# Kernel tuning notes

Hardware: AMD Instinct MI355X
Metric: run time of the kernel (lower is better)

The kernel has to match this reference:

```python
import jax, jax.numpy as jnp
import numpy as np

NUM_EXPERTS = 4


def setup_inputs() -> dict:
    key = jax.random.key(0)
    k1, k2, k3 = jax.random.split(key, 3)
    B, N, H = 8, 2048, 2048
    E = NUM_EXPERTS
    I = H * 4 // E  # expert_intermediate_size = 2048
    x = jax.random.normal(k1, (B, N, H), dtype=jnp.float32)
    gate_up_proj = jax.random.normal(k2, (E, H, 2 * I), dtype=jnp.float32) * 0.02
    down_proj = jax.random.normal(k3, (E, I, H), dtype=jnp.float32) * 0.02
    return {"x": x, "gate_up_proj": gate_up_proj, "down_proj": down_proj}


def reference(x, gate_up_proj, down_proj):
    # Token-routed MLP with deterministic routing: expert(pos) = pos % E.
    # Instead of gathering full weight matrices per token (as the torch code
    # does), group tokens by expert via a reshape: pos = g*E + e -> expert e.
    B, N, H = x.shape
    E, _, two_I = gate_up_proj.shape
    I = two_I // 2
    G = N // E
    x4 = x.reshape(B, G, E, H)
    # gate+up projection, grouped GEMM over expert axis e
    gu = jnp.einsum('bgeh,ehd->bged', x4, gate_up_proj)  # [B,G,E,2I]
    gate, up = gu[..., :I], gu[..., I:]
    inter = jax.nn.silu(gate) * up  # SwiGLU, [B,G,E,I]
    out = jnp.einsum('bgei,eih->bgeh', inter, down_proj)  # [B,G,E,H]
    return out.reshape(B, N, H)
```

## Files before the change

### kernel.cpp

```cpp
#include <hip/hip_runtime.h>

#define HDIM 2048
#define IDIM 2048
#define KD   2048
#define ME   4096
#define NT   64


typedef __bf16 bf16x8 __attribute__((ext_vector_type(8)));
typedef float f32x4 __attribute__((ext_vector_type(4)));

__device__ __forceinline__ unsigned short f2bf(float f) {
  unsigned u = __builtin_bit_cast(unsigned, f);
  u += 0x7FFFu + ((u >> 16) & 1u);
  return (unsigned short)(u >> 16);
}

__device__ __forceinline__ void gld16(const void* g, void* l) {
  __builtin_amdgcn_global_load_lds(
      (const __attribute__((address_space(1))) unsigned int*)g,
      (__attribute__((address_space(3))) unsigned int*)l, 16, 0, 0);
}

template<int N> __device__ __forceinline__ void wait_vmcnt() {
  asm volatile("s_waitcnt vmcnt(%0)" :: "i"(N) : "memory");
}

__global__ void __launch_bounds__(256) pack_x(const float* __restrict__ x,
                                              unsigned short* __restrict__ xb) {
  const int row = blockIdx.x;
  const int n = row & 2047;
  const int b = row >> 11;
  const int e = n & 3, g = n >> 2;
  const float4* src = (const float4*)(x + (size_t)row * HDIM);
  unsigned short* dst = xb + ((size_t)e * ME + b * 512 + g) * HDIM;
  const int t = threadIdx.x;
  float4 v0 = src[2 * t];
  float4 v1 = src[2 * t + 1];
  uint4 pk;
  pk.x = (unsigned)f2bf(v0.x) | ((unsigned)f2bf(v0.y) << 16);
  pk.y = (unsigned)f2bf(v0.z) | ((unsigned)f2bf(v0.w) << 16);
  pk.z = (unsigned)f2bf(v1.x) | ((unsigned)f2bf(v1.y) << 16);
  pk.w = (unsigned)f2bf(v1.z) | ((unsigned)f2bf(v1.w) << 16);
  *(uint4*)(dst + 8 * t) = pk;
}

__global__ void __launch_bounds__(256) transpose_cvt(const float* __restrict__ src,
                                                     unsigned short* __restrict__ dst,
                                                     int R, int C) {
  __shared__ unsigned short tile[32][33];
  const size_t eo = (size_t)blockIdx.z * R * C;
  src += eo;
  dst += eo;
  const int c0 = blockIdx.x * 32, r0 = blockIdx.y * 32;
  const int tx = threadIdx.x & 31, ty = threadIdx.x >> 5;
#pragma unroll
  for (int j = 0; j < 4; ++j) {
    int r = r0 + ty + j * 8;
    tile[ty + j * 8][tx] = f2bf(src[(size_t)r * C + c0 + tx]);
  }
  __syncthreads();
#pragma unroll
  for (int j = 0; j < 4; ++j) {
    int c = c0 + ty + j * 8;
    dst[(size_t)c * R + r0 + tx] = tile[tx][ty + j * 8];
  }
}


template<int VMN, bool STG>
__device__ __forceinline__ void g1_tile(const unsigned short* S, int ab0, int bb0,
                                        const unsigned short*& ap0, const unsigned short*& ap1,
                                        const unsigned short*& bgp, const unsigned short*& bup,
                                        unsigned short* sb,
                                        f32x4 (&accg)[8][2], f32x4 (&accu)[8][2]) {
  wait_vmcnt<VMN>();
  __builtin_amdgcn_s_barrier();
  asm volatile("" ::: "memory");
  bf16x8 a[4], bg[2], bu[2];
#pragma unroll
  for (int i = 0; i < 4; ++i) a[i] = *(const bf16x8*)(S + ab0 + i * 512);
#pragma unroll
  for (int j = 0; j < 2; ++j) {
    bg[j] = *(const bf16x8*)(S + bb0 + j * 512);
    bu[j] = *(const bf16x8*)(S + bb0 + 4096 + j * 512);
  }
  if constexpr (STG) { gld16(ap0, sb); gld16(ap1, sb + 4096); }
  __builtin_amdgcn_s_setprio(1);
#pragma unroll
  for (int i = 0; i < 4; ++i)
#pragma unroll
    for (int j = 0; j < 2; ++j) {
      accg[i][j] = __builtin_amdgcn_mfma_f32_16x16x32_bf16(a[i], bg[j], accg[i][j], 0, 0, 0);
      accu[i][j] = __builtin_amdgcn_mfma_f32_16x16x32_bf16(a[i], bu[j], accu[i][j], 0, 0, 0);
    }
  __builtin_amdgcn_s_setprio(0);
  bf16x8 a2[4];
#pragma unroll
  for (int i = 0; i < 4; ++i) a2[i] = *(const bf16x8*)(S + ab0 + (i + 4) * 512);
  if constexpr (STG) {
    gld16(bgp, sb + 8192); gld16(bup, sb + 12288);
    ap0 += 32; ap1 += 32; bgp += 32; bup += 32;
  }
  __builtin_amdgcn_s_setprio(1);
#pragma unroll
  for (int i = 0; i < 4; ++i)
#pragma unroll
    for (int j = 0; j < 2; ++j) {
      accg[i + 4][j] = __builtin_amdgcn_mfma_f32_16x16x32_bf16(a2[i], bg[j], accg[i + 4][j], 0, 0, 0);
      accu[i + 4][j] = __builtin_amdgcn_mfma_f32_16x16x32_bf16(a2[i], bu[j], accu[i + 4][j], 0, 0, 0);
    }
  __builtin_amdgcn_s_setprio(0);
}

__global__ void __launch_bounds__(512) gemm1_silu(const unsigned short* __restrict__ xb,
                                                  const unsigned short* __restrict__ w1t,
                                                  unsigned short* __restrict__ inter) {
  __shared__ unsigned short SM[65536];
  const int e = blockIdx.z;
  const int m0 = blockIdx.x * 256;
  const int c0 = blockIdx.y * 128;
  const int t = threadIdx.x;
  const int lane = t & 63;
  const int wave = t >> 6;
  const int wm = wave >> 2;
  const int wn = wave & 3;

  const unsigned short* xe = xb + (size_t)e * ME * KD;
  const unsigned short* we = w1t + (size_t)e * 4096 * KD;

  const int srow = t >> 2;
  const int scol = ((t & 3) * 8) ^ ((t & 32) ? 16 : 0);
  const unsigned short* ap0 = xe + (size_t)(m0 + srow) * KD + scol;
  const unsigned short* ap1 = ap0 + (size_t)128 * KD;
  const unsigned short* bgp = we + (size_t)(c0 + srow) * KD + scol;
  const unsigned short* bup = bgp + (size_t)2048 * KD;

  const int l15 = lane & 15;
  const int kqs = ((lane >> 4) * 8) ^ ((lane & 8) ? 16 : 0);
  const int ab0 = (wm * 128 + l15) * 32 + kqs;
  const int bb0 = 8192 + (wn * 32 + l15) * 32 + kqs;

  f32x4 accg[8][2] = {};
  f32x4 accu[8][2] = {};

#pragma unroll
  for (int s = 0; s < 3; ++s) {
    unsigned short* sb = SM + s * 16384 + t * 8;
    gld16(ap0, sb); gld16(ap1, sb + 4096); gld16(bgp, sb + 8192); gld16(bup, sb + 12288);
    ap0 += 32; ap1 += 32; bgp += 32; bup += 32;
  }

#pragma unroll 1
  for (int kt = 0; kt < NT - 3; ++kt)
    g1_tile<8, true>(SM + (kt & 3) * 16384, ab0, bb0, ap0, ap1, bgp, bup,
                     SM + ((kt + 3) & 3) * 16384 + t * 8, accg, accu);
  g1_tile<8, false>(SM + ((NT - 3) & 3) * 16384, ab0, bb0, ap0, ap1, bgp, bup, SM, accg, accu);
  g1_tile<4, false>(SM + ((NT - 2) & 3) * 16384, ab0, bb0, ap0, ap1, bgp, bup, SM, accg, accu);
  g1_tile<0, false>(SM + ((NT - 1) & 3) * 16384, ab0, bb0, ap0, ap1, bgp, bup, SM, accg, accu);

  const int quad = lane >> 4;
#pragma unroll
  for (int i = 0; i < 8; ++i)
#pragma unroll
    for (int j = 0; j < 2; ++j)
#pragma unroll
      for (int r = 0; r < 4; ++r) {
        int row = wm * 128 + i * 16 + quad * 4 + r;
        int col = wn * 32 + j * 16 + l15;
        float g = accg[i][j][r];
        float u = accu[i][j][r];
        float sv = g / (1.0f + __expf(-g));
        SM[row * 136 + col] = f2bf(sv * u);
      }
  __syncthreads();
  unsigned short* ip = inter + ((size_t)e * ME + m0) * IDIM + c0;
#pragma unroll
  for (int p = 0; p < 8; ++p) {
    int idx = p * 512 + t;
    int row = idx >> 4, part = idx & 15;
    *(uint4*)(ip + (size_t)row * IDIM + part * 8) = *(const uint4*)(SM + row * 136 + part * 8);
  }
}

template<int VMN, bool STG>
__device__ __forceinline__ void g2_tile(const unsigned short* S, int ab0, int bb0,
                                        const unsigned short*& ap0, const unsigned short*& ap1,
                                        const unsigned short*& bp0, const unsigned short*& bp1,
                                        unsigned short* sb, f32x4 (&acc)[8][4]) {
  wait_vmcnt<VMN>();
  __builtin_amdgcn_s_barrier();
  asm volatile("" ::: "memory");
  bf16x8 a[4], b[4];
#pragma unroll
  for (int i = 0; i < 4; ++i) a[i] = *(const bf16x8*)(S + ab0 + i * 512);
#pragma unroll
  for (int j = 0; j < 4; ++j) b[j] = *(const bf16x8*)(S + bb0 + j * 512);
  if constexpr (STG) { gld16(ap0, sb); gld16(ap1, sb + 4096); }
  __builtin_amdgcn_s_setprio(1);
#pragma unroll
  for (int i = 0; i < 4; ++i)
#pragma unroll
    for (int j = 0; j < 4; ++j)
      acc[i][j] = __builtin_amdgcn_mfma_f32_16x16x32_bf16(a[i], b[j], acc[i][j], 0, 0, 0);
  __builtin_amdgcn_s_setprio(0);
  bf16x8 a2[4];
#pragma unroll
  for (int i = 0; i < 4; ++i) a2[i] = *(const bf16x8*)(S + ab0 + (i + 4) * 512);
  if constexpr (STG) {
    gld16(bp0, sb + 8192); gld16(bp1, sb + 12288);
    ap0 += 32; ap1 += 32; bp0 += 32; bp1 += 32;
  }
  __builtin_amdgcn_s_setprio(1);
#pragma unroll
  for (int i = 0; i < 4; ++i)
#pragma unroll
    for (int j = 0; j < 4; ++j)
      acc[i + 4][j] = __builtin_amdgcn_mfma_f32_16x16x32_bf16(a2[i], b[j], acc[i + 4][j], 0, 0, 0);
  __builtin_amdgcn_s_setprio(0);
}

__global__ void __launch_bounds__(512) gemm2(const unsigned short* __restrict__ inter,
                                             const unsigned short* __restrict__ w2t,
                                             float* __restrict__ out) {
  __shared__ unsigned short SM[65536];
  const int e = blockIdx.z;
  const int m0 = blockIdx.x * 256;
  const int n0 = blockIdx.y * 256;
  const int t = threadIdx.x;
  const int lane = t & 63;
  const int wave = t >> 6;
  const int wm = wave >> 2;
  const int wn = wave & 3;

  const unsigned short* ae = inter + (size_t)e * ME * IDIM;
  const unsigned short* be = w2t + (size_t)e * HDIM * IDIM;

  const int srow = t >> 2;
  const int scol = ((t & 3) * 8) ^ ((t & 32) ? 16 : 0);
  const unsigned short* ap0 = ae + (size_t)(m0 + srow) * IDIM + scol;
  const unsigned short* ap1 = ap0 + (size_t)128 * IDIM;
  const unsigned short* bp0 = be + (size_t)(n0 + srow) * IDIM + scol;
  const unsigned short* bp1 = bp0 + (size_t)128 * IDIM;

  const int l15 = lane & 15;
  const int kqs = ((lane >> 4) * 8) ^ ((lane & 8) ? 16 : 0);
  const int ab0 = (wm * 128 + l15) * 32 + kqs;
  const int bb0 = 8192 + (wn * 64 + l15) * 32 + kqs;

  f32x4 acc[8][4] = {};

#pragma unroll
  for (int s = 0; s < 3; ++s) {
    unsigned short* sb = SM + s * 16384 + t * 8;
    gld16(ap0, sb); gld16(ap1, sb + 4096); gld16(bp0, sb + 8192); gld16(bp1, sb + 12288);
    ap0 += 32; ap1 += 32; bp0 += 32; bp1 += 32;
  }

#pragma unroll 1
  for (int kt = 0; kt < NT - 3; ++kt)
    g2_tile<8, true>(SM + (kt & 3) * 16384, ab0, bb0, ap0, ap1, bp0, bp1,
                     SM + ((kt + 3) & 3) * 16384 + t * 8, acc);
  g2_tile<8, false>(SM + ((NT - 3) & 3) * 16384, ab0, bb0, ap0, ap1, bp0, bp1, SM, acc);
  g2_tile<4, false>(SM + ((NT - 2) & 3) * 16384, ab0, bb0, ap0, ap1, bp0, bp1, SM, acc);
  g2_tile<0, false>(SM + ((NT - 1) & 3) * 16384, ab0, bb0, ap0, ap1, bp0, bp1, SM, acc);

  const int quad = lane >> 4;
#pragma unroll
  for (int i = 0; i < 8; ++i)
#pragma unroll
    for (int r = 0; r < 4; ++r) {
      int trow = m0 + wm * 128 + i * 16 + quad * 4 + r;
      int b_ = trow >> 9, g_ = trow & 511;
      float* orow = out + ((size_t)((b_ << 11) + (g_ << 2) + e)) * HDIM + n0 + wn * 64;
#pragma unroll
      for (int j = 0; j < 4; ++j) orow[j * 16 + l15] = acc[i][j][r];
    }
}

extern "C" void kernel_launch(void* const* d_in, const int* in_sizes, int n_in,
                              void* d_out, int out_size, void* d_ws, size_t ws_size,
                              hipStream_t stream) {
  (void)in_sizes; (void)n_in; (void)out_size; (void)ws_size;
  const float* x  = (const float*)d_in[0];
  const float* w1 = (const float*)d_in[1];
  const float* w2 = (const float*)d_in[2];
  float* out = (float*)d_out;

  char* ws = (char*)d_ws;
  unsigned short* xb    = (unsigned short*)(ws);
  unsigned short* w1t   = (unsigned short*)(ws + 67108864);
  unsigned short* w2t   = (unsigned short*)(ws + 134217728);
  unsigned short* inter = (unsigned short*)(ws + 167772160);

  pack_x<<<16384, 256, 0, stream>>>(x, xb);
  transpose_cvt<<<dim3(128, 64, 4), 256, 0, stream>>>(w1, w1t, 2048, 4096);
  transpose_cvt<<<dim3(64, 64, 4), 256, 0, stream>>>(w2, w2t, 2048, 2048);
  gemm1_silu<<<dim3(16, 16, 4), 512, 0, stream>>>(xb, w1t, inter);
  gemm2<<<dim3(16, 8, 4), 512, 0, stream>>>(inter, w2t, out);
}
```

Before: 745.2 us.

## Software-pipeline LDS fragment reads across k-tiles in both GEMMs

Reorganizes the inner k-loop of both GEMM kernels so the first A fragments and the B fragments for the next tile are read from LDS during the last MFMA group of the current tile. A fragments are also read in small chunks interleaved between MFMA groups. All four global-to-LDS loads are now issued at the top of each iteration, and the vmcnt wait thresholds are changed to match. The aim is to hide LDS read latency behind MFMAs and shorten the stall after each barrier. In exchange, register pressure rises and correctness depends on the 4-stage buffer ring not being overwritten before the next-tile reads.

```diff
diff --git a/kernel.cpp b/kernel.cpp
--- a/kernel.cpp
+++ b/kernel.cpp
@@ -68,49 +68,66 @@
 }
 
 
-template<int VMN, bool STG>
-__device__ __forceinline__ void g1_tile(const unsigned short* S, int ab0, int bb0,
+template<int BASE>
+__device__ __forceinline__ void g1_mfma8(const bf16x8* ap, const bf16x8 (&bg)[2],
+                                         const bf16x8 (&bu)[2],
+                                         f32x4 (&accg)[8][2], f32x4 (&accu)[8][2]) {
+#pragma unroll
+  for (int k = 0; k < 2; ++k)
+#pragma unroll
+    for (int j = 0; j < 2; ++j) {
+      accg[BASE + k][j] = __builtin_amdgcn_mfma_f32_16x16x32_bf16(ap[k], bg[j], accg[BASE + k][j], 0, 0, 0);
+      accu[BASE + k][j] = __builtin_amdgcn_mfma_f32_16x16x32_bf16(ap[k], bu[j], accu[BASE + k][j], 0, 0, 0);
+    }
+}
+
+template<int VMN, bool STG, bool PRE>
+__device__ __forceinline__ void g1_body(const unsigned short* Scur, const unsigned short* Snxt,
+                                        int ab0, int bb0,
                                         const unsigned short*& ap0, const unsigned short*& ap1,
                                         const unsigned short*& bgp, const unsigned short*& bup,
                                         unsigned short* sb,
+                                        bf16x8 (&a01)[2], bf16x8 (&bg)[2], bf16x8 (&bu)[2],
                                         f32x4 (&accg)[8][2], f32x4 (&accu)[8][2]) {
   wait_vmcnt<VMN>();
   __builtin_amdgcn_s_barrier();
   asm volatile("" ::: "memory");
-  bf16x8 a[4], bg[2], bu[2];
-#pragma unroll
-  for (int i = 0; i < 4; ++i) a[i] = *(const bf16x8*)(S + ab0 + i * 512);
-#pragma unroll
-  for (int j = 0; j < 2; ++j) {
-    bg[j] = *(const bf16x8*)(S + bb0 + j * 512);
-    bu[j] = *(const bf16x8*)(S + bb0 + 4096 + j * 512);
-  }
-  if constexpr (STG) { gld16(ap0, sb); gld16(ap1, sb + 4096); }
-  __builtin_amdgcn_s_setprio(1);
-#pragma unroll
-  for (int i = 0; i < 4; ++i)
-#pragma unroll
-    for (int j = 0; j < 2; ++j) {
-      accg[i][j] = __builtin_amdgcn_mfma_f32_16x16x32_bf16(a[i], bg[j], accg[i][j], 0, 0, 0);
-      accu[i][j] = __builtin_amdgcn_mfma_f32_16x16x32_bf16(a[i], bu[j], accu[i][j], 0, 0, 0);
-    }
-  __builtin_amdgcn_s_setprio(0);
-  bf16x8 a2[4];
-#pragma unroll
-  for (int i = 0; i < 4; ++i) a2[i] = *(const bf16x8*)(S + ab0 + (i + 4) * 512);
   if constexpr (STG) {
-    gld16(bgp, sb + 8192); gld16(bup, sb + 12288);
+    gld16(ap0, sb); gld16(ap1, sb + 4096); gld16(bgp, sb + 8192); gld16(bup, sb + 12288);
     ap0 += 32; ap1 += 32; bgp += 32; bup += 32;
   }
-  __builtin_amdgcn_s_setprio(1);
-#pragma unroll
-  for (int i = 0; i < 4; ++i)
-#pragma unroll
-    for (int j = 0; j < 2; ++j) {
-      accg[i + 4][j] = __builtin_amdgcn_mfma_f32_16x16x32_bf16(a2[i], bg[j], accg[i + 4][j], 0, 0, 0);
-      accu[i + 4][j] = __builtin_amdgcn_mfma_f32_16x16x32_bf16(a2[i], bu[j], accu[i + 4][j], 0, 0, 0);
-    }
-  __builtin_amdgcn_s_setprio(0);
+  bf16x8 a23[2], a45[2], a67[2];
+  a23[0] = *(const bf16x8*)(Scur + ab0 + 2 * 512);
+  a23[1] = *(const bf16x8*)(Scur + ab0 + 3 * 512);
+  __builtin_amdgcn_s_setprio(1);
+  g1_mfma8<0>(a01, bg, bu, accg, accu);
+  __builtin_amdgcn_s_setprio(0);
+  a45[0] = *(const bf16x8*)(Scur + ab0 + 4 * 512);
+  a45[1] = *(const bf16x8*)(Scur + ab0 + 5 * 512);
+  __builtin_amdgcn_s_setprio(1);
+  g1_mfma8<2>(a23, bg, bu, accg, accu);
+  __builtin_amdgcn_s_setprio(0);
+  a67[0] = *(const bf16x8*)(Scur + ab0 + 6 * 512);
+  a67[1] = *(const bf16x8*)(Scur + ab0 + 7 * 512);
+  __builtin_amdgcn_s_setprio(1);
+  g1_mfma8<4>(a45, bg, bu, accg, accu);
+  __builtin_amdgcn_s_setprio(0);
+  bf16x8 bgn[2], bun[2];
+  if constexpr (PRE) {
+    a01[0] = *(const bf16x8*)(Snxt + ab0);
+    a01[1] = *(const bf16x8*)(Snxt + ab0 + 512);
+    bgn[0] = *(const bf16x8*)(Snxt + bb0);
+    bgn[1] = *(const bf16x8*)(Snxt + bb0 + 512);
+    bun[0] = *(const bf16x8*)(Snxt + bb0 + 4096);
+    bun[1] = *(const bf16x8*)(Snxt + bb0 + 4096 + 512);
+  }
+  __builtin_amdgcn_s_setprio(1);
+  g1_mfma8<6>(a67, bg, bu, accg, accu);
+  __builtin_amdgcn_s_setprio(0);
+  if constexpr (PRE) {
+    bg[0] = bgn[0]; bg[1] = bgn[1];
+    bu[0] = bun[0]; bu[1] = bun[1];
+  }
 }
 
 __global__ void __launch_bounds__(512) gemm1_silu(const unsigned short* __restrict__ xb,
@@ -150,14 +167,28 @@
     gld16(ap0, sb); gld16(ap1, sb + 4096); gld16(bgp, sb + 8192); gld16(bup, sb + 12288);
     ap0 += 32; ap1 += 32; bgp += 32; bup += 32;
   }
+  wait_vmcnt<8>();
+  __builtin_amdgcn_s_barrier();
+  asm volatile("" ::: "memory");
+  bf16x8 a01[2], bg[2], bu[2];
+  a01[0] = *(const bf16x8*)(SM + ab0);
+  a01[1] = *(const bf16x8*)(SM + ab0 + 512);
+  bg[0] = *(const bf16x8*)(SM + bb0);
+  bg[1] = *(const bf16x8*)(SM + bb0 + 512);
+  bu[0] = *(const bf16x8*)(SM + bb0 + 4096);
+  bu[1] = *(const bf16x8*)(SM + bb0 + 4096 + 512);
 
 #pragma unroll 1
   for (int kt = 0; kt < NT - 3; ++kt)
-    g1_tile<8, true>(SM + (kt & 3) * 16384, ab0, bb0, ap0, ap1, bgp, bup,
-                     SM + ((kt + 3) & 3) * 16384 + t * 8, accg, accu);
-  g1_tile<8, false>(SM + ((NT - 3) & 3) * 16384, ab0, bb0, ap0, ap1, bgp, bup, SM, accg, accu);
-  g1_tile<4, false>(SM + ((NT - 2) & 3) * 16384, ab0, bb0, ap0, ap1, bgp, bup, SM, accg, accu);
-  g1_tile<0, false>(SM + ((NT - 1) & 3) * 16384, ab0, bb0, ap0, ap1, bgp, bup, SM, accg, accu);
+    g1_body<4, true, true>(SM + (kt & 3) * 16384, SM + ((kt + 1) & 3) * 16384, ab0, bb0,
+                           ap0, ap1, bgp, bup, SM + ((kt + 3) & 3) * 16384 + t * 8,
+                           a01, bg, bu, accg, accu);
+  g1_body<4, false, true>(SM + ((NT - 3) & 3) * 16384, SM + ((NT - 2) & 3) * 16384, ab0, bb0,
+                          ap0, ap1, bgp, bup, SM, a01, bg, bu, accg, accu);
+  g1_body<0, false, true>(SM + ((NT - 2) & 3) * 16384, SM + ((NT - 1) & 3) * 16384, ab0, bb0,
+                          ap0, ap1, bgp, bup, SM, a01, bg, bu, accg, accu);
+  g1_body<0, false, false>(SM + ((NT - 1) & 3) * 16384, SM, ab0, bb0,
+                           ap0, ap1, bgp, bup, SM, a01, bg, bu, accg, accu);
 
   const int quad = lane >> 4;
 #pragma unroll
@@ -183,41 +214,60 @@
   }
 }
 
-template<int VMN, bool STG>
-__device__ __forceinline__ void g2_tile(const unsigned short* S, int ab0, int bb0,
+template<int BASE>
+__device__ __forceinline__ void g2_mfma8(const bf16x8* ap, const bf16x8 (&b)[4],
+                                         f32x4 (&acc)[8][4]) {
+#pragma unroll
+  for (int k = 0; k < 2; ++k)
+#pragma unroll
+    for (int j = 0; j < 4; ++j)
+      acc[BASE + k][j] = __builtin_amdgcn_mfma_f32_16x16x32_bf16(ap[k], b[j], acc[BASE + k][j], 0, 0, 0);
+}
+
+template<int VMN, bool STG, bool PRE>
+__device__ __forceinline__ void g2_body(const unsigned short* Scur, const unsigned short* Snxt,
+                                        int ab0, int bb0,
                                         const unsigned short*& ap0, const unsigned short*& ap1,
                                         const unsigned short*& bp0, const unsigned short*& bp1,
-                                        unsigned short* sb, f32x4 (&acc)[8][4]) {
+                                        unsigned short* sb,
+                                        bf16x8 (&a01)[2], bf16x8 (&b)[4], f32x4 (&acc)[8][4]) {
   wait_vmcnt<VMN>();
   __builtin_amdgcn_s_barrier();
   asm volatile("" ::: "memory");
-  bf16x8 a[4], b[4];
-#pragma unroll
-  for (int i = 0; i < 4; ++i) a[i] = *(const bf16x8*)(S + ab0 + i * 512);
-#pragma unroll
-  for (int j = 0; j < 4; ++j) b[j] = *(const bf16x8*)(S + bb0 + j * 512);
-  if constexpr (STG) { gld16(ap0, sb); gld16(ap1, sb + 4096); }
-  __builtin_amdgcn_s_setprio(1);
-#pragma unroll
-  for (int i = 0; i < 4; ++i)
-#pragma unroll
-    for (int j = 0; j < 4; ++j)
-      acc[i][j] = __builtin_amdgcn_mfma_f32_16x16x32_bf16(a[i], b[j], acc[i][j], 0, 0, 0);
-  __builtin_amdgcn_s_setprio(0);
-  bf16x8 a2[4];
-#pragma unroll
-  for (int i = 0; i < 4; ++i) a2[i] = *(const bf16x8*)(S + ab0 + (i + 4) * 512);
   if constexpr (STG) {
-    gld16(bp0, sb + 8192); gld16(bp1, sb + 12288);
+    gld16(ap0, sb); gld16(ap1, sb + 4096); gld16(bp0, sb + 8192); gld16(bp1, sb + 12288);
     ap0 += 32; ap1 += 32; bp0 += 32; bp1 += 32;
   }
-  __builtin_amdgcn_s_setprio(1);
-#pragma unroll
-  for (int i = 0; i < 4; ++i)
-#pragma unroll
-    for (int j = 0; j < 4; ++j)
-      acc[i + 4][j] = __builtin_amdgcn_mfma_f32_16x16x32_bf16(a2[i], b[j], acc[i + 4][j], 0, 0, 0);
-  __builtin_amdgcn_s_setprio(0);
+  bf16x8 a23[2], a45[2], a67[2];
+  a23[0] = *(const bf16x8*)(Scur + ab0 + 2 * 512);
+  a23[1] = *(const bf16x8*)(Scur + ab0 + 3 * 512);
+  __builtin_amdgcn_s_setprio(1);
+  g2_mfma8<0>(a01, b, acc);
+  __builtin_amdgcn_s_setprio(0);
+  a45[0] = *(const bf16x8*)(Scur + ab0 + 4 * 512);
+  a45[1] = *(const bf16x8*)(Scur + ab0 + 5 * 512);
+  __builtin_amdgcn_s_setprio(1);
+  g2_mfma8<2>(a23, b, acc);
+  __builtin_amdgcn_s_setprio(0);
+  a67[0] = *(const bf16x8*)(Scur + ab0 + 6 * 512);
+  a67[1] = *(const bf16x8*)(Scur + ab0 + 7 * 512);
+  __builtin_amdgcn_s_setprio(1);
+  g2_mfma8<4>(a45, b, acc);
+  __builtin_amdgcn_s_setprio(0);
+  bf16x8 bn[4];
+  if constexpr (PRE) {
+    a01[0] = *(const bf16x8*)(Snxt + ab0);
+    a01[1] = *(const bf16x8*)(Snxt + ab0 + 512);
+#pragma unroll
+    for (int j = 0; j < 4; ++j) bn[j] = *(const bf16x8*)(Snxt + bb0 + j * 512);
+  }
+  __builtin_amdgcn_s_setprio(1);
+  g2_mfma8<6>(a67, b, acc);
+  __builtin_amdgcn_s_setprio(0);
+  if constexpr (PRE) {
+#pragma unroll
+    for (int j = 0; j < 4; ++j) b[j] = bn[j];
+  }
 }
 
 __global__ void __launch_bounds__(512) gemm2(const unsigned short* __restrict__ inter,
@@ -256,14 +306,26 @@
     gld16(ap0, sb); gld16(ap1, sb + 4096); gld16(bp0, sb + 8192); gld16(bp1, sb + 12288);
     ap0 += 32; ap1 += 32; bp0 += 32; bp1 += 32;
   }
+  wait_vmcnt<8>();
+  __builtin_amdgcn_s_barrier();
+  asm volatile("" ::: "memory");
+  bf16x8 a01[2], b[4];
+  a01[0] = *(const bf16x8*)(SM + ab0);
+  a01[1] = *(const bf16x8*)(SM + ab0 + 512);
+#pragma unroll
+  for (int j = 0; j < 4; ++j) b[j] = *(const bf16x8*)(SM + bb0 + j * 512);
 
 #pragma unroll 1
   for (int kt = 0; kt < NT - 3; ++kt)
-    g2_tile<8, true>(SM + (kt & 3) * 16384, ab0, bb0, ap0, ap1, bp0, bp1,
-                     SM + ((kt + 3) & 3) * 16384 + t * 8, acc);
-  g2_tile<8, false>(SM + ((NT - 3) & 3) * 16384, ab0, bb0, ap0, ap1, bp0, bp1, SM, acc);
-  g2_tile<4, false>(SM + ((NT - 2) & 3) * 16384, ab0, bb0, ap0, ap1, bp0, bp1, SM, acc);
-  g2_tile<0, false>(SM + ((NT - 1) & 3) * 16384, ab0, bb0, ap0, ap1, bp0, bp1, SM, acc);
+    g2_body<4, true, true>(SM + (kt & 3) * 16384, SM + ((kt + 1) & 3) * 16384, ab0, bb0,
+                           ap0, ap1, bp0, bp1, SM + ((kt + 3) & 3) * 16384 + t * 8,
+                           a01, b, acc);
+  g2_body<4, false, true>(SM + ((NT - 3) & 3) * 16384, SM + ((NT - 2) & 3) * 16384, ab0, bb0,
+                          ap0, ap1, bp0, bp1, SM, a01, b, acc);
+  g2_body<0, false, true>(SM + ((NT - 2) & 3) * 16384, SM + ((NT - 1) & 3) * 16384, ab0, bb0,
+                          ap0, ap1, bp0, bp1, SM, a01, b, acc);
+  g2_body<0, false, false>(SM + ((NT - 1) & 3) * 16384, SM, ab0, bb0,
+                           ap0, ap1, bp0, bp1, SM, a01, b, acc);
 
   const int quad = lane >> 4;
 #pragma unroll
```

New measurement: 755.5 us. Within noise of the previous version (+1.4%).

## Restructure GEMM mainloops into double-buffered K=64 stages with split barriers

Applied to the files above, without the earlier changes.

Both GEMM kernels replace the 4-stage ring of K=32 LDS tiles with a 2-slot double buffer of K=64 tiles. Each K=64 step runs four MFMA phases, each bracketed by explicit barriers with lgkmcnt waits, and global-to-LDS prefetches for the next slot are interleaved between phases. The goal is to overlap loads with MFMA work at finer granularity and to cut loop iterations. The cost is more barriers per K step and a shallower prefetch depth in K-tiles, which could expose more memory latency.

```diff
diff --git a/kernel.cpp b/kernel.cpp
--- a/kernel.cpp
+++ b/kernel.cpp
@@ -4,7 +4,7 @@
 #define IDIM 2048
 #define KD   2048
 #define ME   4096
-#define NT   64
+#define NT2  32
 
 
 typedef __bf16 bf16x8 __attribute__((ext_vector_type(8)));
@@ -24,6 +24,16 @@
 
 template<int N> __device__ __forceinline__ void wait_vmcnt() {
   asm volatile("s_waitcnt vmcnt(%0)" :: "i"(N) : "memory");
+}
+
+__device__ __forceinline__ void midbar() {
+  __builtin_amdgcn_s_barrier();
+  asm volatile("s_waitcnt lgkmcnt(0)" ::: "memory");
+  __builtin_amdgcn_sched_barrier(0);
+}
+__device__ __forceinline__ void endbar() {
+  __builtin_amdgcn_s_barrier();
+  asm volatile("" ::: "memory");
 }
 
 __global__ void __launch_bounds__(256) pack_x(const float* __restrict__ x,
@@ -68,24 +78,21 @@
 }
 
 
-template<int VMN, bool STG>
-__device__ __forceinline__ void g1_tile(const unsigned short* S, int ab0, int bb0,
-                                        const unsigned short*& ap0, const unsigned short*& ap1,
-                                        const unsigned short*& bgp, const unsigned short*& bup,
-                                        unsigned short* sb,
-                                        f32x4 (&accg)[8][2], f32x4 (&accu)[8][2]) {
-  wait_vmcnt<VMN>();
-  __builtin_amdgcn_s_barrier();
-  asm volatile("" ::: "memory");
+template<bool STG, int VM2, int VM4>
+__device__ __forceinline__ void g1_k64(const unsigned short* S, unsigned short* sb,
+                                       int ab0, int bb0,
+                                       const unsigned short* ap0, const unsigned short* ap1,
+                                       const unsigned short* bgp, const unsigned short* bup,
+                                       f32x4 (&accg)[8][2], f32x4 (&accu)[8][2]) {
   bf16x8 a[4], bg[2], bu[2];
 #pragma unroll
   for (int i = 0; i < 4; ++i) a[i] = *(const bf16x8*)(S + ab0 + i * 512);
-#pragma unroll
-  for (int j = 0; j < 2; ++j) {
-    bg[j] = *(const bf16x8*)(S + bb0 + j * 512);
-    bu[j] = *(const bf16x8*)(S + bb0 + 4096 + j * 512);
-  }
+  bg[0] = *(const bf16x8*)(S + 8192 + bb0);
+  bg[1] = *(const bf16x8*)(S + 8192 + bb0 + 512);
+  bu[0] = *(const bf16x8*)(S + 8192 + bb0 + 4096);
+  bu[1] = *(const bf16x8*)(S + 8192 + bb0 + 4096 + 512);
   if constexpr (STG) { gld16(ap0, sb); gld16(ap1, sb + 4096); }
+  midbar();
   __builtin_amdgcn_s_setprio(1);
 #pragma unroll
   for (int i = 0; i < 4; ++i)
@@ -95,22 +102,55 @@
       accu[i][j] = __builtin_amdgcn_mfma_f32_16x16x32_bf16(a[i], bu[j], accu[i][j], 0, 0, 0);
     }
   __builtin_amdgcn_s_setprio(0);
-  bf16x8 a2[4];
-#pragma unroll
-  for (int i = 0; i < 4; ++i) a2[i] = *(const bf16x8*)(S + ab0 + (i + 4) * 512);
-  if constexpr (STG) {
-    gld16(bgp, sb + 8192); gld16(bup, sb + 12288);
-    ap0 += 32; ap1 += 32; bgp += 32; bup += 32;
-  }
+  endbar();
+#pragma unroll
+  for (int i = 0; i < 4; ++i) a[i] = *(const bf16x8*)(S + ab0 + (i + 4) * 512);
+  if constexpr (STG) { gld16(bgp, sb + 8192); gld16(bup, sb + 12288); }
+  wait_vmcnt<VM2>();
+  midbar();
   __builtin_amdgcn_s_setprio(1);
 #pragma unroll
   for (int i = 0; i < 4; ++i)
 #pragma unroll
     for (int j = 0; j < 2; ++j) {
-      accg[i + 4][j] = __builtin_amdgcn_mfma_f32_16x16x32_bf16(a2[i], bg[j], accg[i + 4][j], 0, 0, 0);
-      accu[i + 4][j] = __builtin_amdgcn_mfma_f32_16x16x32_bf16(a2[i], bu[j], accu[i + 4][j], 0, 0, 0);
-    }
-  __builtin_amdgcn_s_setprio(0);
+      accg[i + 4][j] = __builtin_amdgcn_mfma_f32_16x16x32_bf16(a[i], bg[j], accg[i + 4][j], 0, 0, 0);
+      accu[i + 4][j] = __builtin_amdgcn_mfma_f32_16x16x32_bf16(a[i], bu[j], accu[i + 4][j], 0, 0, 0);
+    }
+  __builtin_amdgcn_s_setprio(0);
+  endbar();
+#pragma unroll
+  for (int i = 0; i < 4; ++i) a[i] = *(const bf16x8*)(S + 16384 + ab0 + i * 512);
+  bg[0] = *(const bf16x8*)(S + 24576 + bb0);
+  bg[1] = *(const bf16x8*)(S + 24576 + bb0 + 512);
+  bu[0] = *(const bf16x8*)(S + 24576 + bb0 + 4096);
+  bu[1] = *(const bf16x8*)(S + 24576 + bb0 + 4096 + 512);
+  if constexpr (STG) { gld16(ap0 + 32, sb + 16384); gld16(ap1 + 32, sb + 20480); }
+  midbar();
+  __builtin_amdgcn_s_setprio(1);
+#pragma unroll
+  for (int i = 0; i < 4; ++i)
+#pragma unroll
+    for (int j = 0; j < 2; ++j) {
+      accg[i][j] = __builtin_amdgcn_mfma_f32_16x16x32_bf16(a[i], bg[j], accg[i][j], 0, 0, 0);
+      accu[i][j] = __builtin_amdgcn_mfma_f32_16x16x32_bf16(a[i], bu[j], accu[i][j], 0, 0, 0);
+    }
+  __builtin_amdgcn_s_setprio(0);
+  endbar();
+#pragma unroll
+  for (int i = 0; i < 4; ++i) a[i] = *(const bf16x8*)(S + 16384 + ab0 + (i + 4) * 512);
+  if constexpr (STG) { gld16(bgp + 32, sb + 24576); gld16(bup + 32, sb + 28672); }
+  wait_vmcnt<VM4>();
+  midbar();
+  __builtin_amdgcn_s_setprio(1);
+#pragma unroll
+  for (int i = 0; i < 4; ++i)
+#pragma unroll
+    for (int j = 0; j < 2; ++j) {
+      accg[i + 4][j] = __builtin_amdgcn_mfma_f32_16x16x32_bf16(a[i], bg[j], accg[i + 4][j], 0, 0, 0);
+      accu[i + 4][j] = __builtin_amdgcn_mfma_f32_16x16x32_bf16(a[i], bu[j], accu[i + 4][j], 0, 0, 0);
+    }
+  __builtin_amdgcn_s_setprio(0);
+  endbar();
 }
 
 __global__ void __launch_bounds__(512) gemm1_silu(const unsigned short* __restrict__ xb,
@@ -139,25 +179,30 @@
   const int l15 = lane & 15;
   const int kqs = ((lane >> 4) * 8) ^ ((lane & 8) ? 16 : 0);
   const int ab0 = (wm * 128 + l15) * 32 + kqs;
-  const int bb0 = 8192 + (wn * 32 + l15) * 32 + kqs;
+  const int bb0 = (wn * 32 + l15) * 32 + kqs;
 
   f32x4 accg[8][2] = {};
   f32x4 accu[8][2] = {};
 
-#pragma unroll
-  for (int s = 0; s < 3; ++s) {
-    unsigned short* sb = SM + s * 16384 + t * 8;
-    gld16(ap0, sb); gld16(ap1, sb + 4096); gld16(bgp, sb + 8192); gld16(bup, sb + 12288);
-    ap0 += 32; ap1 += 32; bgp += 32; bup += 32;
-  }
+  {
+    unsigned short* sb = SM + t * 8;
+    gld16(ap0, sb);        gld16(ap1, sb + 4096);
+    gld16(bgp, sb + 8192); gld16(bup, sb + 12288);
+    gld16(ap0 + 32, sb + 16384); gld16(ap1 + 32, sb + 20480);
+    gld16(bgp + 32, sb + 24576); gld16(bup + 32, sb + 28672);
+  }
+  wait_vmcnt<4>();
+  __builtin_amdgcn_s_barrier();
+  asm volatile("" ::: "memory");
 
 #pragma unroll 1
-  for (int kt = 0; kt < NT - 3; ++kt)
-    g1_tile<8, true>(SM + (kt & 3) * 16384, ab0, bb0, ap0, ap1, bgp, bup,
-                     SM + ((kt + 3) & 3) * 16384 + t * 8, accg, accu);
-  g1_tile<8, false>(SM + ((NT - 3) & 3) * 16384, ab0, bb0, ap0, ap1, bgp, bup, SM, accg, accu);
-  g1_tile<4, false>(SM + ((NT - 2) & 3) * 16384, ab0, bb0, ap0, ap1, bgp, bup, SM, accg, accu);
-  g1_tile<0, false>(SM + ((NT - 1) & 3) * 16384, ab0, bb0, ap0, ap1, bgp, bup, SM, accg, accu);
+  for (int kt = 0; kt < NT2 - 1; ++kt) {
+    ap0 += 64; ap1 += 64; bgp += 64; bup += 64;
+    g1_k64<true, 4, 4>(SM + (kt & 1) * 32768, SM + ((kt + 1) & 1) * 32768 + t * 8,
+                       ab0, bb0, ap0, ap1, bgp, bup, accg, accu);
+  }
+  g1_k64<false, 0, 0>(SM + ((NT2 - 1) & 1) * 32768, SM, ab0, bb0,
+                      ap0, ap1, bgp, bup, accg, accu);
 
   const int quad = lane >> 4;
 #pragma unroll
@@ -183,20 +228,19 @@
   }
 }
 
-template<int VMN, bool STG>
-__device__ __forceinline__ void g2_tile(const unsigned short* S, int ab0, int bb0,
-                                        const unsigned short*& ap0, const unsigned short*& ap1,
-                                        const unsigned short*& bp0, const unsigned short*& bp1,
-                                        unsigned short* sb, f32x4 (&acc)[8][4]) {
-  wait_vmcnt<VMN>();
-  __builtin_amdgcn_s_barrier();
-  asm volatile("" ::: "memory");
+template<bool STG, int VM2, int VM4>
+__device__ __forceinline__ void g2_k64(const unsigned short* S, unsigned short* sb,
+                                       int ab0, int bb0,
+                                       const unsigned short* ap0, const unsigned short* ap1,
+                                       const unsigned short* bp0, const unsigned short* bp1,
+                                       f32x4 (&acc)[8][4]) {
   bf16x8 a[4], b[4];
 #pragma unroll
   for (int i = 0; i < 4; ++i) a[i] = *(const bf16x8*)(S + ab0 + i * 512);
 #pragma unroll
-  for (int j = 0; j < 4; ++j) b[j] = *(const bf16x8*)(S + bb0 + j * 512);
+  for (int j = 0; j < 4; ++j) b[j] = *(const bf16x8*)(S + 8192 + bb0 + j * 512);
   if constexpr (STG) { gld16(ap0, sb); gld16(ap1, sb + 4096); }
+  midbar();
   __builtin_amdgcn_s_setprio(1);
 #pragma unroll
   for (int i = 0; i < 4; ++i)
@@ -204,20 +248,47 @@
     for (int j = 0; j < 4; ++j)
       acc[i][j] = __builtin_amdgcn_mfma_f32_16x16x32_bf16(a[i], b[j], acc[i][j], 0, 0, 0);
   __builtin_amdgcn_s_setprio(0);
-  bf16x8 a2[4];
-#pragma unroll
-  for (int i = 0; i < 4; ++i) a2[i] = *(const bf16x8*)(S + ab0 + (i + 4) * 512);
-  if constexpr (STG) {
-    gld16(bp0, sb + 8192); gld16(bp1, sb + 12288);
-    ap0 += 32; ap1 += 32; bp0 += 32; bp1 += 32;
-  }
+  endbar();
+#pragma unroll
+  for (int i = 0; i < 4; ++i) a[i] = *(const bf16x8*)(S + ab0 + (i + 4) * 512);
+  if constexpr (STG) { gld16(bp0, sb + 8192); gld16(bp1, sb + 12288); }
+  wait_vmcnt<VM2>();
+  midbar();
   __builtin_amdgcn_s_setprio(1);
 #pragma unroll
   for (int i = 0; i < 4; ++i)
 #pragma unroll
     for (int j = 0; j < 4; ++j)
-      acc[i + 4][j] = __builtin_amdgcn_mfma_f32_16x16x32_bf16(a2[i], b[j], acc[i + 4][j], 0, 0, 0);
-  __builtin_amdgcn_s_setprio(0);
+      acc[i + 4][j] = __builtin_amdgcn_mfma_f32_16x16x32_bf16(a[i], b[j], acc[i + 4][j], 0, 0, 0);
+  __builtin_amdgcn_s_setprio(0);
+  endbar();
+#pragma unroll
+  for (int i = 0; i < 4; ++i) a[i] = *(const bf16x8*)(S + 16384 + ab0 + i * 512);
+#pragma unroll
+  for (int j = 0; j < 4; ++j) b[j] = *(const bf16x8*)(S + 24576 + bb0 + j * 512);
+  if constexpr (STG) { gld16(ap0 + 32, sb + 16384); gld16(ap1 + 32, sb + 20480); }
+  midbar();
+  __builtin_amdgcn_s_setprio(1);
+#pragma unroll
+  for (int i = 0; i < 4; ++i)
+#pragma unroll
+    for (int j = 0; j < 4; ++j)
+      acc[i][j] = __builtin_amdgcn_mfma_f32_16x16x32_bf16(a[i], b[j], acc[i][j], 0, 0, 0);
+  __builtin_amdgcn_s_setprio(0);
+  endbar();
+#pragma unroll
+  for (int i = 0; i < 4; ++i) a[i] = *(const bf16x8*)(S + 16384 + ab0 + (i + 4) * 512);
+  if constexpr (STG) { gld16(bp0 + 32, sb + 24576); gld16(bp1 + 32, sb + 28672); }
+  wait_vmcnt<VM4>();
+  midbar();
+  __builtin_amdgcn_s_setprio(1);
+#pragma unroll
+  for (int i = 0; i < 4; ++i)
+#pragma unroll
+    for (int j = 0; j < 4; ++j)
+      acc[i + 4][j] = __builtin_amdgcn_mfma_f32_16x16x32_bf16(a[i], b[j], acc[i + 4][j], 0, 0, 0);
+  __builtin_amdgcn_s_setprio(0);
+  endbar();
 }
 
 __global__ void __launch_bounds__(512) gemm2(const unsigned short* __restrict__ inter,
@@ -246,24 +317,29 @@
   const int l15 = lane & 15;
   const int kqs = ((lane >> 4) * 8) ^ ((lane & 8) ? 16 : 0);
   const int ab0 = (wm * 128 + l15) * 32 + kqs;
-  const int bb0 = 8192 + (wn * 64 + l15) * 32 + kqs;
+  const int bb0 = (wn * 64 + l15) * 32 + kqs;
 
   f32x4 acc[8][4] = {};
 
-#pragma unroll
-  for (int s = 0; s < 3; ++s) {
-    unsigned short* sb = SM + s * 16384 + t * 8;
-    gld16(ap0, sb); gld16(ap1, sb + 4096); gld16(bp0, sb + 8192); gld16(bp1, sb + 12288);
-    ap0 += 32; ap1 += 32; bp0 += 32; bp1 += 32;
-  }
+  {
+    unsigned short* sb = SM + t * 8;
+    gld16(ap0, sb);        gld16(ap1, sb + 4096);
+    gld16(bp0, sb + 8192); gld16(bp1, sb + 12288);
+    gld16(ap0 + 32, sb + 16384); gld16(ap1 + 32, sb + 20480);
+    gld16(bp0 + 32, sb + 24576); gld16(bp1 + 32, sb + 28672);
+  }
+  wait_vmcnt<4>();
+  __builtin_amdgcn_s_barrier();
+  asm volatile("" ::: "memory");
 
 #pragma unroll 1
-  for (int kt = 0; kt < NT - 3; ++kt)
-    g2_tile<8, true>(SM + (kt & 3) * 16384, ab0, bb0, ap0, ap1, bp0, bp1,
-                     SM + ((kt + 3) & 3) * 16384 + t * 8, acc);
-  g2_tile<8, false>(SM + ((NT - 3) & 3) * 16384, ab0, bb0, ap0, ap1, bp0, bp1, SM, acc);
-  g2_tile<4, false>(SM + ((NT - 2) & 3) * 16384, ab0, bb0, ap0, ap1, bp0, bp1, SM, acc);
-  g2_tile<0, false>(SM + ((NT - 1) & 3) * 16384, ab0, bb0, ap0, ap1, bp0, bp1, SM, acc);
+  for (int kt = 0; kt < NT2 - 1; ++kt) {
+    ap0 += 64; ap1 += 64; bp0 += 64; bp1 += 64;
+    g2_k64<true, 4, 4>(SM + (kt & 1) * 32768, SM + ((kt + 1) & 1) * 32768 + t * 8,
+                       ab0, bb0, ap0, ap1, bp0, bp1, acc);
+  }
+  g2_k64<false, 0, 0>(SM + ((NT2 - 1) & 1) * 32768, SM, ab0, bb0,
+                      ap0, ap1, bp0, bp1, acc);
 
   const int quad = lane >> 4;
 #pragma unroll
```

Measured after the change: 749.1 us. Within noise of the previous version (+0.5%).
